# Optimization experiments

Measured on AMD Instinct MI355X. Metric: run time of the kernel, lower is better.

Reference implementation:

```python
import jax, jax.numpy as jnp
import numpy as np

B, T, N, V, C, E = 64, 100, 25, 128, 128, 64
EPS = 1e-5


def setup_inputs() -> dict:
    key = jax.random.key(0)
    ks = jax.random.split(key, 6)
    x = jax.random.normal(ks[0], (B, T, N, V), jnp.float32)
    edge_index = jax.random.randint(ks[1], (2, E), 0, N, dtype=jnp.int64)
    W1 = jax.random.normal(ks[2], (V, C), jnp.float32) * (1.0 / np.sqrt(V))
    b1 = jnp.zeros((C,), jnp.float32)
    W2 = jax.random.normal(ks[3], (C, C), jnp.float32) * (1.0 / np.sqrt(C))
    b2 = jnp.zeros((C,), jnp.float32)
    gamma = jnp.ones((T,), jnp.float32)
    beta = jnp.zeros((T,), jnp.float32)
    return {"x": x, "edge_index": edge_index, "W1": W1, "b1": b1,
            "W2": W2, "b2": b2, "gamma": gamma, "beta": beta}


def _gcn_norm(edge_index, n):
    # GCNConv default: add self-loops, symmetric D^{-1/2} A_hat D^{-1/2} norm.
    loop = jnp.arange(n, dtype=edge_index.dtype)
    src = jnp.concatenate([edge_index[0], loop])  # [E + N]
    tgt = jnp.concatenate([edge_index[1], loop])
    deg = jnp.zeros((n,), jnp.float32).at[tgt].add(1.0)
    dis = jax.lax.rsqrt(deg)  # deg >= 1 due to self-loops
    return src, tgt, dis[src] * dis[tgt]


def _gcn_layer(h, W, b, src, tgt, norm):
    # h: [G, N, Cin] -> [G, N, Cout]; linear then gather-scale-scatter aggregate.
    h = jnp.einsum('gnc,cd->gnd', h, W)
    msg = h[:, src, :] * norm[None, :, None]          # [G, E+N, Cout]
    out = jnp.zeros_like(h).at[:, tgt, :].add(msg)    # scatter-add to targets
    return out + b


def reference(x, edge_index, W1, b1, W2, b2, gamma, beta):
    Bv, Tv, Nv, Vv = x.shape
    h = x.reshape(Bv * Tv, Nv, Vv)  # B*T independent graphs, shared edge_index
    src, tgt, norm = _gcn_norm(edge_index, Nv)
    h = _gcn_layer(h, W1, b1, src, tgt, norm)
    h = _gcn_layer(h, W2, b2, src, tgt, norm)
    y = h.reshape(Bv, Tv, Nv, -1)
    # BatchNorm2d(T) in training mode: batch stats over (B, N, C) per T-channel.
    mean = y.mean(axis=(0, 2, 3), keepdims=True)
    var = y.var(axis=(0, 2, 3), keepdims=True)  # biased, matches torch normalization
    y = (y - mean) * jax.lax.rsqrt(var + EPS)
    y = y * gamma[None, :, None, None] + beta[None, :, None, None]
    return jax.nn.relu(y)
```

## Files before the change

### kernel.cpp

```cpp
#include <hip/hip_runtime.h>

#define T_DIM   100
#define N_NODES 25
#define C_DIM   128
#define B_DIM   64
#define G_TOTAL 6400
#define GNV     3200
#define CNT_PER_T 204800.0f

#define WS_A2P  0
#define WS_RS1  640
#define WS_BW   768
#define WS_SUM  1024
#define WS_SSQ  1152
#define WS_W12T 2048

#define YSTR  36
#define YGSTR (128 * YSTR)

typedef __attribute__((ext_vector_type(8))) short short8;
typedef __attribute__((ext_vector_type(4))) float f32x4;

__device__ __forceinline__ unsigned short f2bf(float f) {
  unsigned int u = __float_as_uint(f);
  u += 0x7FFFu + ((u >> 16) & 1u);
  return (unsigned short)(u >> 16);
}
__device__ __forceinline__ unsigned int pack2bf(float a, float b) {
  return (unsigned int)f2bf(a) | ((unsigned int)f2bf(b) << 16);
}

__global__ void k_pre(const int* __restrict__ edge, const float* __restrict__ W1,
                      const float* __restrict__ W2, const float* __restrict__ b1,
                      float* __restrict__ wsf) {
  __shared__ float sA[N_NODES * N_NODES];
  __shared__ float sA2[N_NODES * N_NODES];
  __shared__ float sdeg[N_NODES];
  __shared__ float sdis[N_NODES];
  const int tid = threadIdx.x;

  if (blockIdx.x < 64) {
    int j = blockIdx.x * 256 + tid;
    int c = j & 127, v = j >> 7;
    float acc = 0.f;
#pragma unroll 8
    for (int u = 0; u < 128; u++) acc = fmaf(W1[v * 128 + u], W2[u * 128 + c], acc);
    ((unsigned short*)(wsf + WS_W12T))[c * 128 + v] = f2bf(acc);
    if (j < 128) {
      float a2 = 0.f;
      for (int u = 0; u < 128; u++) a2 = fmaf(W2[u * 128 + j], b1[u], a2);
      wsf[WS_BW + j] = a2;
    }
    return;
  }

  if (tid < N_NODES) sdeg[tid] = 0.f;
  for (int j = tid; j < N_NODES * N_NODES; j += 256) sA[j] = 0.f;
  __syncthreads();
  if (tid < 64) atomicAdd(&sdeg[edge[64 + tid]], 1.f);
  __syncthreads();
  if (tid < N_NODES) sdis[tid] = rsqrtf(sdeg[tid] + 1.f);
  __syncthreads();
  if (tid < 64) {
    int s = edge[tid], tg = edge[64 + tid];
    atomicAdd(&sA[tg * N_NODES + s], sdis[s] * sdis[tg]);
  }
  __syncthreads();
  if (tid < N_NODES) atomicAdd(&sA[tid * N_NODES + tid], sdis[tid] * sdis[tid]);
  __syncthreads();
  for (int j = tid; j < N_NODES * N_NODES; j += 256) {
    int n = j / N_NODES, m = j - n * N_NODES;
    float acc = 0.f;
    for (int k = 0; k < N_NODES; k++) acc = fmaf(sA[n * N_NODES + k], sA[k * N_NODES + m], acc);
    sA2[j] = acc;
  }
  __syncthreads();
  for (int j = tid; j < 1024; j += 256) {
    int m = j >> 5, k = j & 31;
    float v = (m < N_NODES && k < N_NODES) ? sA2[m * N_NODES + k] : 0.f;
    ((unsigned short*)(wsf + WS_A2P))[j] = f2bf(v);
  }
  if (tid < N_NODES) {
    float rs = 0.f;
    for (int m = 0; m < N_NODES; m++) rs += sA[tid * N_NODES + m];
    wsf[WS_RS1 + tid] = rs;
  }
  if (tid < T_DIM) { wsf[WS_SUM + tid] = 0.f; wsf[WS_SSQ + tid] = 0.f; }
}

__global__ __launch_bounds__(256, 4) void k_main(const float* __restrict__ x,
                                                 const float* __restrict__ b2,
                                                 const float* __restrict__ wsc,
                                                 float* __restrict__ stats,
                                                 float* __restrict__ out) {
  __shared__ __align__(16) unsigned short LB[4 * YGSTR];
  __shared__ float sBW[128];
  __shared__ float sB2[128];
  __shared__ float rs1[32];
  __shared__ float red[8];
  const int tid = threadIdx.x;
  const int bid = blockIdx.x;
  const int t = bid % T_DIM;
  const int bq = bid / T_DIM;
  const int wv = tid >> 6, lane = tid & 63, quad = lane >> 4, l16 = lane & 15;

  if (tid < 128) {
    sBW[tid] = wsc[WS_BW + tid];
    if (tid < N_NODES) rs1[tid] = wsc[WS_RS1 + tid];
  } else {
    sB2[tid - 128] = b2[tid - 128];
  }
  for (int j = tid; j < 12 * 128; j += 256) {
    int pr = j >> 7;
    int g = pr >> 2, rr = pr & 3;
    g = pr / 3; rr = pr - g * 3;
    LB[(g * 28 + 25 + rr) * 128 + (j & 127)] = 0;
  }

  {
    const int v = tid & 127;
    const int gl0 = tid >> 7;
    const int g0 = (bq * 4 + gl0) * T_DIM + t;
    const float* xp0 = x + g0 * GNV + v;
    const float* xp1 = xp0 + 2 * T_DIM * GNV;
    float x0[25], x1[25];
#pragma unroll
    for (int m = 0; m < 25; m++) { x0[m] = xp0[m * 128]; x1[m] = xp1[m * 128]; }
#pragma unroll
    for (int n = 0; n < 25; n++) {
      int r0 = gl0 * 28 + n, r1 = (gl0 + 2) * 28 + n;
      LB[r0 * 128 + (v ^ ((r0 & 15) << 3))] = f2bf(x0[n]);
      LB[r1 * 128 + (v ^ ((r1 & 15) << 3))] = f2bf(x1[n]);
    }
  }

  short8 bfr[2][4];
  {
    const unsigned short* Wg = (const unsigned short*)(wsc + WS_W12T);
#pragma unroll
    for (int nt = 0; nt < 2; nt++) {
      const short8* rp = (const short8*)&Wg[(wv * 32 + nt * 16 + l16) * 128];
#pragma unroll
      for (int ks = 0; ks < 4; ks++) bfr[nt][ks] = rp[(ks << 2) | quad];
    }
  }
  __syncthreads();

  f32x4 acc[7][2];
#pragma unroll
  for (int mt = 0; mt < 7; mt++)
#pragma unroll
    for (int nt = 0; nt < 2; nt++)
#pragma unroll
      for (int r = 0; r < 4; r++) acc[mt][nt][r] = 0.f;

#pragma unroll
  for (int ks = 0; ks < 4; ks++) {
    const int cc = (ks << 2) | quad;
#pragma unroll
    for (int mt = 0; mt < 7; mt++) {
      int arow = mt * 16 + l16;
      short8 afr = *(const short8*)&LB[arow * 128 + ((cc ^ (arow & 15)) << 3)];
#pragma unroll
      for (int nt = 0; nt < 2; nt++)
        acc[mt][nt] = __builtin_amdgcn_mfma_f32_16x16x32_bf16(afr, bfr[nt][ks], acc[mt][nt], 0, 0, 0);
    }
  }
  __syncthreads();

#pragma unroll
  for (int mt = 0; mt < 7; mt++) {
    int row0 = mt * 16 + quad * 4;
    int g = row0 / 28;
    int rl = row0 - g * 28;
#pragma unroll
    for (int nt = 0; nt < 2; nt++) {
      int c = wv * 32 + nt * 16 + l16;
      uint2 p;
      p.x = pack2bf(acc[mt][nt][0], acc[mt][nt][1]);
      p.y = pack2bf(acc[mt][nt][2], acc[mt][nt][3]);
      *(uint2*)&LB[g * YGSTR + c * YSTR + rl] = p;
    }
  }
  {
    uint2 z; z.x = 0u; z.y = 0u;
    for (int j = tid; j < 512; j += 256) {
      int g = j >> 7, c = j & 127;
      *(uint2*)&LB[g * YGSTR + c * YSTR + 28] = z;
    }
  }
  __syncthreads();

  const unsigned short* A2p = (const unsigned short*)(wsc + WS_A2P);
  short8 a2f[2];
#pragma unroll
  for (int mt2 = 0; mt2 < 2; mt2++)
    a2f[mt2] = *(const short8*)&A2p[(mt2 * 16 + l16) * 32 + quad * 8];

  const int obase = ((bq * 4 + wv) * T_DIM + t) * GNV;
  float sum = 0.f, ssq = 0.f;
#pragma unroll
  for (int half = 0; half < 2; half++) {
    f32x4 acc2[2][4];
#pragma unroll
    for (int mt2 = 0; mt2 < 2; mt2++)
#pragma unroll
      for (int nt = 0; nt < 4; nt++)
#pragma unroll
        for (int r = 0; r < 4; r++) acc2[mt2][nt][r] = 0.f;

#pragma unroll
    for (int nt = 0; nt < 4; nt++) {
      int c = (half * 4 + nt) * 16 + l16;
      int base = wv * YGSTR + c * YSTR + quad * 8;
      uint2 lo = *(const uint2*)&LB[base];
      uint2 hi = *(const uint2*)&LB[base + 4];
      uint4 w; w.x = lo.x; w.y = lo.y; w.z = hi.x; w.w = hi.y;
      short8 bf = __builtin_bit_cast(short8, w);
#pragma unroll
      for (int mt2 = 0; mt2 < 2; mt2++)
        acc2[mt2][nt] = __builtin_amdgcn_mfma_f32_16x16x32_bf16(a2f[mt2], bf, acc2[mt2][nt], 0, 0, 0);
    }
#pragma unroll
    for (int mt2 = 0; mt2 < 2; mt2++) {
#pragma unroll
      for (int nt = 0; nt < 4; nt++) {
        int c = (half * 4 + nt) * 16 + l16;
        float bw = sBW[c], bb = sB2[c];
#pragma unroll
        for (int r = 0; r < 4; r++) {
          int m = mt2 * 16 + quad * 4 + r;
          if (m < N_NODES) {
            float v = acc2[mt2][nt][r] + rs1[m] * bw + bb;
            out[obase + m * 128 + c] = v;
            sum += v;
            ssq += v * v;
          }
        }
      }
    }
  }

#pragma unroll
  for (int off = 32; off > 0; off >>= 1) {
    sum += __shfl_down(sum, off, 64);
    ssq += __shfl_down(ssq, off, 64);
  }
  if (lane == 0) { red[wv] = sum; red[4 + wv] = ssq; }
  __syncthreads();
  if (tid == 0) {
    atomicAdd(&stats[t], red[0] + red[1] + red[2] + red[3]);
    atomicAdd(&stats[128 + t], red[4] + red[5] + red[6] + red[7]);
  }
}

#define NORM_STR  1280000
__global__ __launch_bounds__(256) void k_norm(float* __restrict__ out,
                                              const float* __restrict__ stats,
                                              const float* __restrict__ gamma,
                                              const float* __restrict__ beta) {
  const int i0 = blockIdx.x * 256 + threadIdx.x;
  const float inv = 1.f / CNT_PER_T;
  float4 h[4];
  float g[4], bb[4];
  int base[4];
#pragma unroll
  for (int k = 0; k < 4; k++) {
    int i4 = i0 + k * NORM_STR;
    base[k] = i4 * 4;
    int t = (base[k] / GNV) % T_DIM;
    float s = stats[t], q = stats[128 + t];
    float mean = s * inv;
    float var = fmaf(q, inv, -mean * mean);
    float rstd = rsqrtf(var + 1e-5f);
    g[k] = gamma[t] * rstd;
    bb[k] = fmaf(-mean, g[k], beta[t]);
    h[k] = *(const float4*)(out + base[k]);
  }
#pragma unroll
  for (int k = 0; k < 4; k++) {
    float4 v = h[k];
    v.x = fmaxf(fmaf(v.x, g[k], bb[k]), 0.f);
    v.y = fmaxf(fmaf(v.y, g[k], bb[k]), 0.f);
    v.z = fmaxf(fmaf(v.z, g[k], bb[k]), 0.f);
    v.w = fmaxf(fmaf(v.w, g[k], bb[k]), 0.f);
    *(float4*)(out + base[k]) = v;
  }
}

extern "C" void kernel_launch(void* const* d_in, const int* in_sizes, int n_in,
                              void* d_out, int out_size, void* d_ws, size_t ws_size,
                              hipStream_t stream) {
  const float* x     = (const float*)d_in[0];
  const int*   edge  = (const int*)d_in[1];
  const float* W1    = (const float*)d_in[2];
  const float* b1    = (const float*)d_in[3];
  const float* W2    = (const float*)d_in[4];
  const float* b2    = (const float*)d_in[5];
  const float* gamma = (const float*)d_in[6];
  const float* beta  = (const float*)d_in[7];
  float* out = (float*)d_out;
  float* wsf = (float*)d_ws;

  k_pre<<<65, 256, 0, stream>>>(edge, W1, W2, b1, wsf);
  k_main<<<G_TOTAL / 4, 256, 0, stream>>>(x, b2, wsf, wsf + WS_SUM, out);
  k_norm<<<NORM_STR / 256, 256, 0, stream>>>(out, wsf + WS_SUM, gamma, beta);
}
```

Measured before the change: 200.8 us.

## Fuse batchnorm into main kernel via persistent blocks and grid barrier

Drops the separate normalization kernel. Each of 800 blocks now processes two graph units, keeps its pre-norm outputs in registers as packed bf16, and waits at a global atomic barrier for the per-T statistics. It then applies the affine normalization and ReLU and writes the output once. This removes one full write-then-read pass over the output and a kernel launch. In exchange it adds register pressure, an extra bf16 rounding of the pre-norm values, and it relies on all 800 blocks being resident at the same time, or the barrier deadlocks.

New measurement: 369.9 us. 1.84x slower.

```diff
diff --git a/kernel.cpp b/kernel.cpp
--- a/kernel.cpp
+++ b/kernel.cpp
@@ -7,12 +7,14 @@
 #define G_TOTAL 6400
 #define GNV     3200
 #define CNT_PER_T 204800.0f
+#define NBLOCKS 800
 
 #define WS_A2P  0
 #define WS_RS1  640
 #define WS_BW   768
 #define WS_SUM  1024
 #define WS_SSQ  1152
+#define WS_BAR  1472
 #define WS_W12T 2048
 
 #define YSTR  36
@@ -29,6 +31,8 @@
 __device__ __forceinline__ unsigned int pack2bf(float a, float b) {
   return (unsigned int)f2bf(a) | ((unsigned int)f2bf(b) << 16);
 }
+__device__ __forceinline__ float bf_lo(unsigned int p) { return __uint_as_float(p << 16); }
+__device__ __forceinline__ float bf_hi(unsigned int p) { return __uint_as_float(p & 0xFFFF0000u); }
 
 __global__ void k_pre(const int* __restrict__ edge, const float* __restrict__ W1,
                       const float* __restrict__ W2, const float* __restrict__ b1,
@@ -85,14 +89,18 @@
     for (int m = 0; m < N_NODES; m++) rs += sA[tid * N_NODES + m];
     wsf[WS_RS1 + tid] = rs;
   }
-  if (tid < T_DIM) { wsf[WS_SUM + tid] = 0.f; wsf[WS_SSQ + tid] = 0.f; }
+  if (tid < T_DIM) { wsf[WS_SUM + tid] = 0.f; wsf[WS_SSQ - WS_SUM + WS_SUM + tid] = 0.f; }
+  if (tid < T_DIM) wsf[WS_SSQ + tid] = 0.f;
+  if (tid == 0) *(unsigned int*)(wsf + WS_BAR) = 0u;
 }
 
 __global__ __launch_bounds__(256, 4) void k_main(const float* __restrict__ x,
                                                  const float* __restrict__ b2,
                                                  const float* __restrict__ wsc,
                                                  float* __restrict__ stats,
-                                                 float* __restrict__ out) {
+                                                 float* __restrict__ out,
+                                                 const float* __restrict__ gamma,
+                                                 const float* __restrict__ beta) {
   __shared__ __align__(16) unsigned short LB[4 * YGSTR];
   __shared__ float sBW[128];
   __shared__ float sB2[128];
@@ -100,38 +108,13 @@
   __shared__ float red[8];
   const int tid = threadIdx.x;
   const int bid = blockIdx.x;
-  const int t = bid % T_DIM;
-  const int bq = bid / T_DIM;
   const int wv = tid >> 6, lane = tid & 63, quad = lane >> 4, l16 = lane & 15;
 
   if (tid < 128) {
     sBW[tid] = wsc[WS_BW + tid];
-    if (tid < N_NODES) rs1[tid] = wsc[WS_RS1 + tid];
+    if (tid < 32) rs1[tid] = (tid < N_NODES) ? wsc[WS_RS1 + tid] : 0.f;
   } else {
     sB2[tid - 128] = b2[tid - 128];
-  }
-  for (int j = tid; j < 12 * 128; j += 256) {
-    int pr = j >> 7;
-    int g = pr >> 2, rr = pr & 3;
-    g = pr / 3; rr = pr - g * 3;
-    LB[(g * 28 + 25 + rr) * 128 + (j & 127)] = 0;
-  }
-
-  {
-    const int v = tid & 127;
-    const int gl0 = tid >> 7;
-    const int g0 = (bq * 4 + gl0) * T_DIM + t;
-    const float* xp0 = x + g0 * GNV + v;
-    const float* xp1 = xp0 + 2 * T_DIM * GNV;
-    float x0[25], x1[25];
-#pragma unroll
-    for (int m = 0; m < 25; m++) { x0[m] = xp0[m * 128]; x1[m] = xp1[m * 128]; }
-#pragma unroll
-    for (int n = 0; n < 25; n++) {
-      int r0 = gl0 * 28 + n, r1 = (gl0 + 2) * 28 + n;
-      LB[r0 * 128 + (v ^ ((r0 & 15) << 3))] = f2bf(x0[n]);
-      LB[r1 * 128 + (v ^ ((r1 & 15) << 3))] = f2bf(x1[n]);
-    }
   }
 
   short8 bfr[2][4];
@@ -144,147 +127,202 @@
       for (int ks = 0; ks < 4; ks++) bfr[nt][ks] = rp[(ks << 2) | quad];
     }
   }
-  __syncthreads();
-
-  f32x4 acc[7][2];
-#pragma unroll
-  for (int mt = 0; mt < 7; mt++)
-#pragma unroll
-    for (int nt = 0; nt < 2; nt++)
-#pragma unroll
-      for (int r = 0; r < 4; r++) acc[mt][nt][r] = 0.f;
-
-#pragma unroll
-  for (int ks = 0; ks < 4; ks++) {
-    const int cc = (ks << 2) | quad;
-#pragma unroll
-    for (int mt = 0; mt < 7; mt++) {
-      int arow = mt * 16 + l16;
-      short8 afr = *(const short8*)&LB[arow * 128 + ((cc ^ (arow & 15)) << 3)];
-#pragma unroll
-      for (int nt = 0; nt < 2; nt++)
-        acc[mt][nt] = __builtin_amdgcn_mfma_f32_16x16x32_bf16(afr, bfr[nt][ks], acc[mt][nt], 0, 0, 0);
-    }
-  }
-  __syncthreads();
-
-#pragma unroll
-  for (int mt = 0; mt < 7; mt++) {
-    int row0 = mt * 16 + quad * 4;
-    int g = row0 / 28;
-    int rl = row0 - g * 28;
-#pragma unroll
-    for (int nt = 0; nt < 2; nt++) {
-      int c = wv * 32 + nt * 16 + l16;
-      uint2 p;
-      p.x = pack2bf(acc[mt][nt][0], acc[mt][nt][1]);
-      p.y = pack2bf(acc[mt][nt][2], acc[mt][nt][3]);
-      *(uint2*)&LB[g * YGSTR + c * YSTR + rl] = p;
-    }
-  }
-  {
-    uint2 z; z.x = 0u; z.y = 0u;
-    for (int j = tid; j < 512; j += 256) {
-      int g = j >> 7, c = j & 127;
-      *(uint2*)&LB[g * YGSTR + c * YSTR + 28] = z;
-    }
-  }
-  __syncthreads();
-
   const unsigned short* A2p = (const unsigned short*)(wsc + WS_A2P);
   short8 a2f[2];
 #pragma unroll
   for (int mt2 = 0; mt2 < 2; mt2++)
     a2f[mt2] = *(const short8*)&A2p[(mt2 * 16 + l16) * 32 + quad * 8];
 
-  const int obase = ((bq * 4 + wv) * T_DIM + t) * GNV;
-  float sum = 0.f, ssq = 0.f;
-#pragma unroll
-  for (int half = 0; half < 2; half++) {
-    f32x4 acc2[2][4];
-#pragma unroll
-    for (int mt2 = 0; mt2 < 2; mt2++)
-#pragma unroll
-      for (int nt = 0; nt < 4; nt++)
-#pragma unroll
-        for (int r = 0; r < 4; r++) acc2[mt2][nt][r] = 0.f;
-
-#pragma unroll
-    for (int nt = 0; nt < 4; nt++) {
-      int c = (half * 4 + nt) * 16 + l16;
-      int base = wv * YGSTR + c * YSTR + quad * 8;
-      uint2 lo = *(const uint2*)&LB[base];
-      uint2 hi = *(const uint2*)&LB[base + 4];
-      uint4 w; w.x = lo.x; w.y = lo.y; w.z = hi.x; w.w = hi.y;
-      short8 bf = __builtin_bit_cast(short8, w);
+  unsigned int Hp[2][32];
+
+#pragma unroll
+  for (int u = 0; u < 2; u++) {
+    const int unit = bid * 2 + u;
+    const int t = unit % T_DIM;
+    const int bq = unit / T_DIM;
+
+    __syncthreads();
+
+    for (int j = tid; j < 12 * 128; j += 256) {
+      int pr = j >> 7;
+      int g = pr / 3, rr = pr - g * 3;
+      LB[(g * 28 + 25 + rr) * 128 + (j & 127)] = 0;
+    }
+    {
+      const int v = tid & 127;
+      const int gl0 = tid >> 7;
+      const int g0 = (bq * 4 + gl0) * T_DIM + t;
+      const float* xp0 = x + g0 * GNV + v;
+      const float* xp1 = xp0 + 2 * T_DIM * GNV;
+      float x0[25], x1[25];
+#pragma unroll
+      for (int m = 0; m < 25; m++) { x0[m] = xp0[m * 128]; x1[m] = xp1[m * 128]; }
+#pragma unroll
+      for (int n = 0; n < 25; n++) {
+        int r0 = gl0 * 28 + n, r1 = (gl0 + 2) * 28 + n;
+        LB[r0 * 128 + (v ^ ((r0 & 15) << 3))] = f2bf(x0[n]);
+        LB[r1 * 128 + (v ^ ((r1 & 15) << 3))] = f2bf(x1[n]);
+      }
+    }
+    __syncthreads();
+
+    f32x4 acc[7][2];
+#pragma unroll
+    for (int mt = 0; mt < 7; mt++)
+#pragma unroll
+      for (int nt = 0; nt < 2; nt++)
+#pragma unroll
+        for (int r = 0; r < 4; r++) acc[mt][nt][r] = 0.f;
+
+#pragma unroll
+    for (int ks = 0; ks < 4; ks++) {
+      const int cc = (ks << 2) | quad;
+#pragma unroll
+      for (int mt = 0; mt < 7; mt++) {
+        int arow = mt * 16 + l16;
+        short8 afr = *(const short8*)&LB[arow * 128 + ((cc ^ (arow & 15)) << 3)];
+#pragma unroll
+        for (int nt = 0; nt < 2; nt++)
+          acc[mt][nt] = __builtin_amdgcn_mfma_f32_16x16x32_bf16(afr, bfr[nt][ks], acc[mt][nt], 0, 0, 0);
+      }
+    }
+    __syncthreads();
+
+#pragma unroll
+    for (int mt = 0; mt < 7; mt++) {
+      int row0 = mt * 16 + quad * 4;
+      int g = row0 / 28;
+      int rl = row0 - g * 28;
+#pragma unroll
+      for (int nt = 0; nt < 2; nt++) {
+        int c = wv * 32 + nt * 16 + l16;
+        uint2 p;
+        p.x = pack2bf(acc[mt][nt][0], acc[mt][nt][1]);
+        p.y = pack2bf(acc[mt][nt][2], acc[mt][nt][3]);
+        *(uint2*)&LB[g * YGSTR + c * YSTR + rl] = p;
+      }
+    }
+    {
+      uint2 z; z.x = 0u; z.y = 0u;
+      for (int j = tid; j < 512; j += 256) {
+        int g = j >> 7, c = j & 127;
+        *(uint2*)&LB[g * YGSTR + c * YSTR + 28] = z;
+      }
+    }
+    __syncthreads();
+
+    float sum = 0.f, ssq = 0.f;
+#pragma unroll
+    for (int half = 0; half < 2; half++) {
+      f32x4 acc2[2][4];
 #pragma unroll
       for (int mt2 = 0; mt2 < 2; mt2++)
-        acc2[mt2][nt] = __builtin_amdgcn_mfma_f32_16x16x32_bf16(a2f[mt2], bf, acc2[mt2][nt], 0, 0, 0);
-    }
-#pragma unroll
-    for (int mt2 = 0; mt2 < 2; mt2++) {
+#pragma unroll
+        for (int nt = 0; nt < 4; nt++)
+#pragma unroll
+          for (int r = 0; r < 4; r++) acc2[mt2][nt][r] = 0.f;
+
 #pragma unroll
       for (int nt = 0; nt < 4; nt++) {
         int c = (half * 4 + nt) * 16 + l16;
-        float bw = sBW[c], bb = sB2[c];
-#pragma unroll
-        for (int r = 0; r < 4; r++) {
-          int m = mt2 * 16 + quad * 4 + r;
-          if (m < N_NODES) {
-            float v = acc2[mt2][nt][r] + rs1[m] * bw + bb;
-            out[obase + m * 128 + c] = v;
-            sum += v;
-            ssq += v * v;
+        int base = wv * YGSTR + c * YSTR + quad * 8;
+        uint2 lo = *(const uint2*)&LB[base];
+        uint2 hi = *(const uint2*)&LB[base + 4];
+        uint4 w; w.x = lo.x; w.y = lo.y; w.z = hi.x; w.w = hi.y;
+        short8 bf = __builtin_bit_cast(short8, w);
+#pragma unroll
+        for (int mt2 = 0; mt2 < 2; mt2++)
+          acc2[mt2][nt] = __builtin_amdgcn_mfma_f32_16x16x32_bf16(a2f[mt2], bf, acc2[mt2][nt], 0, 0, 0);
+      }
+#pragma unroll
+      for (int mt2 = 0; mt2 < 2; mt2++) {
+#pragma unroll
+        for (int nt = 0; nt < 4; nt++) {
+          int c = (half * 4 + nt) * 16 + l16;
+          float bw = sBW[c], bb = sB2[c];
+          float v[4];
+#pragma unroll
+          for (int r = 0; r < 4; r++) {
+            int m = mt2 * 16 + quad * 4 + r;
+            v[r] = acc2[mt2][nt][r] + rs1[m & 31] * bw + bb;
+            if (m < N_NODES) { sum += v[r]; ssq += v[r] * v[r]; }
           }
+          int bi = ((half * 2 + mt2) * 4 + nt) * 2;
+          Hp[u][bi]     = pack2bf(v[0], v[1]);
+          Hp[u][bi + 1] = pack2bf(v[2], v[3]);
         }
       }
     }
-  }
-
-#pragma unroll
-  for (int off = 32; off > 0; off >>= 1) {
-    sum += __shfl_down(sum, off, 64);
-    ssq += __shfl_down(ssq, off, 64);
-  }
-  if (lane == 0) { red[wv] = sum; red[4 + wv] = ssq; }
-  __syncthreads();
-  if (tid == 0) {
-    atomicAdd(&stats[t], red[0] + red[1] + red[2] + red[3]);
-    atomicAdd(&stats[128 + t], red[4] + red[5] + red[6] + red[7]);
-  }
-}
-
-#define NORM_STR  1280000
-__global__ __launch_bounds__(256) void k_norm(float* __restrict__ out,
-                                              const float* __restrict__ stats,
-                                              const float* __restrict__ gamma,
-                                              const float* __restrict__ beta) {
-  const int i0 = blockIdx.x * 256 + threadIdx.x;
+
+#pragma unroll
+    for (int off = 32; off > 0; off >>= 1) {
+      sum += __shfl_down(sum, off, 64);
+      ssq += __shfl_down(ssq, off, 64);
+    }
+    if (lane == 0) { red[wv] = sum; red[4 + wv] = ssq; }
+    __syncthreads();
+    if (tid == 0) {
+      atomicAdd(&stats[t], red[0] + red[1] + red[2] + red[3]);
+      atomicAdd(&stats[128 + t], red[4] + red[5] + red[6] + red[7]);
+    }
+  }
+
+  {
+    unsigned int* bar = (unsigned int*)(stats + (WS_BAR - WS_SUM));
+    __syncthreads();
+    if (tid == 0) {
+      __hip_atomic_fetch_add(bar, 1u, __ATOMIC_ACQ_REL, __HIP_MEMORY_SCOPE_AGENT);
+      while (__hip_atomic_load(bar, __ATOMIC_ACQUIRE, __HIP_MEMORY_SCOPE_AGENT) < NBLOCKS)
+        __builtin_amdgcn_s_sleep(2);
+    }
+    __syncthreads();
+  }
+
+  {
+    const int t0 = (bid * 2) % T_DIM;
+    const int t1 = (bid * 2 + 1) % T_DIM;
+    if (tid == 0) {
+      red[0] = __hip_atomic_load(&stats[t0],       __ATOMIC_RELAXED, __HIP_MEMORY_SCOPE_AGENT);
+      red[1] = __hip_atomic_load(&stats[128 + t0], __ATOMIC_RELAXED, __HIP_MEMORY_SCOPE_AGENT);
+      red[2] = __hip_atomic_load(&stats[t1],       __ATOMIC_RELAXED, __HIP_MEMORY_SCOPE_AGENT);
+      red[3] = __hip_atomic_load(&stats[128 + t1], __ATOMIC_RELAXED, __HIP_MEMORY_SCOPE_AGENT);
+    }
+    __syncthreads();
+  }
+
   const float inv = 1.f / CNT_PER_T;
-  float4 h[4];
-  float g[4], bb[4];
-  int base[4];
-#pragma unroll
-  for (int k = 0; k < 4; k++) {
-    int i4 = i0 + k * NORM_STR;
-    base[k] = i4 * 4;
-    int t = (base[k] / GNV) % T_DIM;
-    float s = stats[t], q = stats[128 + t];
+#pragma unroll
+  for (int u = 0; u < 2; u++) {
+    const int unit = bid * 2 + u;
+    const int t = unit % T_DIM;
+    const int bq = unit / T_DIM;
+    float s = red[u * 2], q = red[u * 2 + 1];
     float mean = s * inv;
     float var = fmaf(q, inv, -mean * mean);
     float rstd = rsqrtf(var + 1e-5f);
-    g[k] = gamma[t] * rstd;
-    bb[k] = fmaf(-mean, g[k], beta[t]);
-    h[k] = *(const float4*)(out + base[k]);
-  }
-#pragma unroll
-  for (int k = 0; k < 4; k++) {
-    float4 v = h[k];
-    v.x = fmaxf(fmaf(v.x, g[k], bb[k]), 0.f);
-    v.y = fmaxf(fmaf(v.y, g[k], bb[k]), 0.f);
-    v.z = fmaxf(fmaf(v.z, g[k], bb[k]), 0.f);
-    v.w = fmaxf(fmaf(v.w, g[k], bb[k]), 0.f);
-    *(float4*)(out + base[k]) = v;
+    float gg = gamma[t] * rstd;
+    float bbb = fmaf(-mean, gg, beta[t]);
+    const int obase = ((bq * 4 + wv) * T_DIM + t) * GNV;
+#pragma unroll
+    for (int half = 0; half < 2; half++) {
+#pragma unroll
+      for (int mt2 = 0; mt2 < 2; mt2++) {
+#pragma unroll
+        for (int nt = 0; nt < 4; nt++) {
+          int c = (half * 4 + nt) * 16 + l16;
+          int bi = ((half * 2 + mt2) * 4 + nt) * 2;
+          float v[4];
+          v[0] = bf_lo(Hp[u][bi]);     v[1] = bf_hi(Hp[u][bi]);
+          v[2] = bf_lo(Hp[u][bi + 1]); v[3] = bf_hi(Hp[u][bi + 1]);
+#pragma unroll
+          for (int r = 0; r < 4; r++) {
+            int m = mt2 * 16 + quad * 4 + r;
+            if (m < N_NODES)
+              out[obase + m * 128 + c] = fmaxf(fmaf(v[r], gg, bbb), 0.f);
+          }
+        }
+      }
+    }
   }
 }
 
@@ -301,8 +339,8 @@
   const float* beta  = (const float*)d_in[7];
   float* out = (float*)d_out;
   float* wsf = (float*)d_ws;
+  float* stats = wsf + WS_SUM;
 
   k_pre<<<65, 256, 0, stream>>>(edge, W1, W2, b1, wsf);
-  k_main<<<G_TOTAL / 4, 256, 0, stream>>>(x, b2, wsf, wsf + WS_SUM, out);
-  k_norm<<<NORM_STR / 256, 256, 0, stream>>>(out, wsf + WS_SUM, gamma, beta);
-}
+  k_main<<<NBLOCKS, 256, 0, stream>>>(x, b2, wsf, stats, out, gamma, beta);
+}
```
